# Performance work log

Measured on AMD Instinct MI355X. Metric: run time of the kernel, lower is better.

The kernel has to match this reference:

```python
import jax, jax.numpy as jnp
import numpy as np
import math

B, S = 512, 50
L, U = 40000, 20000
D_MODEL, D_LOC, D_USR, D_T, H, D_FF = 80, 56, 12, 12, 4, 160
DH = D_MODEL // H


def _layernorm(x, g, b, eps=1e-5):
    m = x.mean(-1, keepdims=True)
    v = ((x - m) ** 2).mean(-1, keepdims=True)
    return (x - m) / jnp.sqrt(v + eps) * g + b


def setup_inputs() -> dict:
    key = jax.random.key(0)
    ks = jax.random.split(key, 16)
    loc_seq = jax.random.randint(ks[0], (B, S), 0, L)
    user_seq = jax.random.randint(ks[1], (B, S), 0, U)
    weekday_seq = jax.random.randint(ks[2], (B, S), 0, 7)
    start_min_seq = jax.random.uniform(ks[3], (B, S), jnp.float32, 0.0, 1440.0)
    dur_seq = jax.random.uniform(ks[4], (B, S), jnp.float32, 0.0, 600.0)
    diff_seq = jax.random.randint(ks[5], (B, S), 0, 7)
    mask = jnp.ones((B, S), dtype=bool)
    # sinusoidal positional-encoding buffer (60, 80), as in __init__
    pos = np.arange(60, dtype=np.float32)[:, None]
    div = np.exp(np.arange(0, D_MODEL, 2, dtype=np.float32) * (-math.log(10000.0) / D_MODEL))
    pe = np.zeros((60, D_MODEL), dtype=np.float32)
    pe[:, 0::2] = np.sin(pos * div)
    pe[:, 1::2] = np.cos(pos * div)
    g = lambda k, shape: jax.random.normal(k, shape, jnp.float32) * 0.02
    return dict(
        loc_seq=loc_seq, user_seq=user_seq, weekday_seq=weekday_seq,
        start_min_seq=start_min_seq, dur_seq=dur_seq, diff_seq=diff_seq, mask=mask,
        loc_emb=jax.random.normal(ks[6], (L, D_LOC), jnp.float32) * 0.01,
        user_emb=jax.random.normal(ks[7], (U, D_USR), jnp.float32) * 0.01,
        tproj_w=g(ks[8], (6, D_T)), tproj_b=jnp.zeros((D_T,), jnp.float32),
        in_norm_g=jnp.ones((D_MODEL,), jnp.float32), in_norm_b=jnp.zeros((D_MODEL,), jnp.float32),
        attn_in_w=g(ks[9], (3 * D_MODEL, D_MODEL)), attn_in_b=jnp.zeros((3 * D_MODEL,), jnp.float32),
        attn_out_w=g(ks[10], (D_MODEL, D_MODEL)), attn_out_b=jnp.zeros((D_MODEL,), jnp.float32),
        norm1_g=jnp.ones((D_MODEL,), jnp.float32), norm1_b=jnp.zeros((D_MODEL,), jnp.float32),
        ff_w1=g(ks[11], (D_MODEL, D_FF)), ff_b1=jnp.zeros((D_FF,), jnp.float32),
        ff_w2=g(ks[12], (D_FF, D_MODEL)), ff_b2=jnp.zeros((D_MODEL,), jnp.float32),
        norm2_g=jnp.ones((D_MODEL,), jnp.float32), norm2_b=jnp.zeros((D_MODEL,), jnp.float32),
        pred_w1=g(ks[13], (D_MODEL, D_FF)), pred_b1=jnp.zeros((D_FF,), jnp.float32),
        pred_w2=g(ks[14], (D_FF, L)), pred_b2=jnp.zeros((L,), jnp.float32),
        recency_decay=jnp.float32(0.62), freq_weight=jnp.float32(2.2),
        history_scale=jnp.float32(11.0), model_weight=jnp.float32(0.22),
        pe=jnp.asarray(pe),
    )


def _history_scores(loc_seq, mask, recency_decay, freq_weight, history_scale):
    # Vectorized scatter-max (recency) + scatter-add (frequency) over the whole
    # (B, S) index set -- replaces the per-timestep python loop of the original.
    maskf = mask.astype(jnp.float32)
    time_from_end = jnp.arange(S - 1, -1, -1, dtype=jnp.float32)  # seq_len - t - 1
    rw = jnp.power(recency_decay, time_from_end)[None, :] * maskf  # (B, S)
    bidx = jnp.broadcast_to(jnp.arange(B)[:, None], (B, S))
    rec = jnp.zeros((B, L), jnp.float32).at[bidx, loc_seq].max(rw)
    freq = jnp.zeros((B, L), jnp.float32).at[bidx, loc_seq].add(maskf)
    freq = freq / jnp.clip(freq.max(axis=1, keepdims=True), 1.0)
    return history_scale * (rec + freq_weight * freq)


def _forward(loc_seq, user_seq, weekday_seq, start_min_seq, dur_seq, diff_seq, mask,
             loc_emb, user_emb, tproj_w, tproj_b, in_norm_g, in_norm_b,
             attn_in_w, attn_in_b, attn_out_w, attn_out_b, norm1_g, norm1_b,
             ff_w1, ff_b1, ff_w2, ff_b2, norm2_g, norm2_b,
             pred_w1, pred_b1, pred_w2, pred_b2,
             recency_decay, freq_weight, history_scale, model_weight, pe):
    hist = _history_scores(loc_seq, mask, recency_decay, freq_weight, history_scale)
    le = loc_emb[loc_seq]                       # (B, S, 56)
    ue = user_emb[user_seq]                     # (B, S, 12)
    tr = (start_min_seq / 60.0) / 24.0 * 2.0 * jnp.pi
    wr = weekday_seq.astype(jnp.float32) / 7.0 * 2.0 * jnp.pi
    tf = jnp.stack([jnp.sin(tr), jnp.cos(tr), jnp.log1p(dur_seq) / 8.0,
                    jnp.sin(wr), jnp.cos(wr), diff_seq.astype(jnp.float32) / 7.0], axis=-1)
    te = tf @ tproj_w + tproj_b                 # (B, S, 12)
    x = jnp.concatenate([le, ue, te], axis=-1)  # (B, S, 80)
    x = _layernorm(x, in_norm_g, in_norm_b)
    x = x + pe[:S][None]
    # multi-head self-attention with key padding mask (dropout=eval mode)
    qkv = x @ attn_in_w.T + attn_in_b
    q, k, v = jnp.split(qkv, 3, axis=-1)
    q = q.reshape(B, S, H, DH)
    k = k.reshape(B, S, H, DH)
    v = v.reshape(B, S, H, DH)
    scores = jnp.einsum('bqhd,bkhd->bhqk', q, k) / jnp.sqrt(jnp.float32(DH))
    scores = jnp.where(mask[:, None, None, :], scores, -jnp.inf)
    attn = jax.nn.softmax(scores, axis=-1)
    ao = jnp.einsum('bhqk,bkhd->bqhd', attn, v).reshape(B, S, D_MODEL)
    ao = ao @ attn_out_w.T + attn_out_b
    x = _layernorm(x + ao, norm1_g, norm1_b)
    ff = jax.nn.gelu(x @ ff_w1 + ff_b1, approximate=False) @ ff_w2 + ff_b2
    x = _layernorm(x + ff, norm2_g, norm2_b)
    seq_lens = mask.sum(axis=1) - 1             # index of last valid token
    last = jnp.take_along_axis(x, seq_lens[:, None, None], axis=1)[:, 0]  # (B, 80)
    logits = jax.nn.gelu(last @ pred_w1 + pred_b1, approximate=False) @ pred_w2 + pred_b2
    return hist + model_weight * (jax.nn.softmax(logits, axis=1) * L)


def reference(loc_seq, user_seq, weekday_seq, start_min_seq, dur_seq, diff_seq, mask,
              loc_emb, user_emb, tproj_w, tproj_b, in_norm_g, in_norm_b,
              attn_in_w, attn_in_b, attn_out_w, attn_out_b, norm1_g, norm1_b,
              ff_w1, ff_b1, ff_w2, ff_b2, norm2_g, norm2_b,
              pred_w1, pred_b1, pred_w2, pred_b2,
              recency_decay, freq_weight, history_scale, model_weight, pe):
    return _forward(loc_seq, user_seq, weekday_seq, start_min_seq, dur_seq, diff_seq, mask,
                    loc_emb, user_emb, tproj_w, tproj_b, in_norm_g, in_norm_b,
                    attn_in_w, attn_in_b, attn_out_w, attn_out_b, norm1_g, norm1_b,
                    ff_w1, ff_b1, ff_w2, ff_b2, norm2_g, norm2_b,
                    pred_w1, pred_b1, pred_w2, pred_b2,
                    recency_decay, freq_weight, history_scale, model_weight, pe)
```

## Files before the change

kernel.cpp:

```cpp
#include <hip/hip_runtime.h>
#include <math.h>

#define BB 512
#define SS 50
#define LL 40000
#define DM 80
#define DLOC 56
#define DUSR 12
#define HH 4
#define DH 20
#define DFF 160

typedef __attribute__((ext_vector_type(8))) short short8v;
typedef __attribute__((ext_vector_type(4))) float f32x4;

__device__ __forceinline__ unsigned short f2bf(float f) {
    unsigned u = __float_as_uint(f);
    u += 0x7fffu + ((u >> 16) & 1u);
    return (unsigned short)(u >> 16);
}

__device__ __forceinline__ float gelu_exact(float x) {
    return 0.5f * x * (1.0f + erff(x * 0.70710678118654752f));
}

__global__ __launch_bounds__(256) void k_fused(
        const int* __restrict__ loc_seq, const int* __restrict__ user_seq,
        const int* __restrict__ wd_seq, const float* __restrict__ start_seq,
        const float* __restrict__ dur_seq, const int* __restrict__ diff_seq,
        const float* __restrict__ loc_emb, const float* __restrict__ user_emb,
        const float* __restrict__ tproj_w, const float* __restrict__ tproj_b,
        const float* __restrict__ in_g, const float* __restrict__ in_b,
        const float* __restrict__ pe,
        const float* __restrict__ Wqkv, const float* __restrict__ bqkv,
        const float* __restrict__ aw, const float* __restrict__ ab,
        const float* __restrict__ n1g, const float* __restrict__ n1b,
        const float* __restrict__ w1, const float* __restrict__ b1,
        const float* __restrict__ w2, const float* __restrict__ b2,
        const float* __restrict__ n2g, const float* __restrict__ n2b,
        const float* __restrict__ pw1, const float* __restrict__ pb1,
        const float* __restrict__ p_decay, const float* __restrict__ p_fw,
        const float* __restrict__ p_hs,
        float* __restrict__ histval, int* __restrict__ histloc,
        unsigned short* __restrict__ gvec, float* __restrict__ rowsum) {
    int b = blockIdx.x, tid = threadIdx.x;
    int w = tid >> 6, ln = tid & 63;
    __shared__ __align__(16) float xs[SS][DM];
    __shared__ float xsT[DM][SS];
    __shared__ float tf6[SS][6];
    __shared__ float rw[SS];
    __shared__ int   loc[SS];
    __shared__ int   usr[SS];
    __shared__ float qr[DM];
    __shared__ float uu[HH][DM];
    __shared__ float scw[HH][SS];
    __shared__ float wsm[HH][DM];
    __shared__ float ao[DM];
    __shared__ float v1[DM];
    __shared__ float v2[DM];
    __shared__ float f1[DFF];
    __shared__ float stat[2];

    if (tid == 0) rowsum[b] = 0.f;

    if (tid < SS) {
        int t = tid;
        loc[t] = loc_seq[b * SS + t];
        usr[t] = user_seq[b * SS + t];
        float tr = start_seq[b * SS + t] * (float)(M_PI / 720.0);
        float wrd = (float)wd_seq[b * SS + t] * (float)(2.0 * M_PI / 7.0);
        tf6[t][0] = sinf(tr); tf6[t][1] = cosf(tr);
        tf6[t][2] = log1pf(dur_seq[b * SS + t]) * 0.125f;
        tf6[t][3] = sinf(wrd); tf6[t][4] = cosf(wrd);
        tf6[t][5] = (float)diff_seq[b * SS + t] * (1.f / 7.f);
        rw[t] = exp2f((float)(SS - 1 - t) * log2f(p_decay[0]));
    }
    __syncthreads();

    for (int idx = tid; idx < SS * DM; idx += 256) {
        int t = idx / DM, d = idx - t * DM;
        float v;
        if (d < DLOC) {
            v = loc_emb[(size_t)loc[t] * DLOC + d];
        } else if (d < DLOC + DUSR) {
            v = user_emb[(size_t)usr[t] * DUSR + (d - DLOC)];
        } else {
            int j = d - (DLOC + DUSR);
            float a = tproj_b[j];
            #pragma unroll
            for (int i = 0; i < 6; ++i) a += tf6[t][i] * tproj_w[i * 12 + j];
            v = a;
        }
        xs[t][d] = v;
    }
    __syncthreads();

    for (int t = w; t < SS; t += 4) {
        float a0 = xs[t][ln];
        float a1 = (ln < 16) ? xs[t][64 + ln] : 0.f;
        float sm = a0 + a1;
        #pragma unroll
        for (int m = 1; m < 64; m <<= 1) sm += __shfl_xor(sm, m);
        float mean = sm * (1.f / DM);
        float d0 = a0 - mean, d1 = (ln < 16) ? (a1 - mean) : 0.f;
        float vs = d0 * d0 + d1 * d1;
        #pragma unroll
        for (int m = 1; m < 64; m <<= 1) vs += __shfl_xor(vs, m);
        float inv = rsqrtf(vs * (1.f / DM) + 1e-5f);
        float r0 = d0 * inv * in_g[ln] + in_b[ln] + pe[t * DM + ln];
        xs[t][ln] = r0; xsT[ln][t] = r0;
        if (ln < 16) {
            float r1 = d1 * inv * in_g[64 + ln] + in_b[64 + ln] + pe[t * DM + 64 + ln];
            xs[t][64 + ln] = r1; xsT[64 + ln][t] = r1;
        }
    }
    __syncthreads();

    if (w == 0) {
        int t = ln;
        int c = 0; float rmx = 0.f; int first = (t < SS) ? 1 : 0;
        if (t < SS) {
            int my = loc[t];
            for (int j = 0; j < SS; ++j) {
                if (loc[j] == my) {
                    c++; rmx = fmaxf(rmx, rw[j]);
                    if (j < t) first = 0;
                }
            }
        }
        int mc = c;
        #pragma unroll
        for (int m = 1; m < 64; m <<= 1) mc = max(mc, __shfl_xor(mc, m));
        if (t < SS) {
            float val = 0.f;
            if (first) val = p_hs[0] * (rmx + p_fw[0] * ((float)c / (float)max(mc, 1)));
            histval[b * SS + t] = val;
            histloc[b * SS + t] = loc[t];
        }
    } else if (tid >= 64 && tid < 64 + DM) {
        int j = tid - 64;
        const float* Wr = Wqkv + (size_t)j * DM;
        float a = bqkv[j];
        for (int d = 0; d < DM; ++d) a += xs[49][d] * Wr[d];
        qr[j] = a;
    }
    __syncthreads();

    {
        int idx = tid;
        float a0 = 0.f, a1 = 0.f;
        int h0 = idx / DM, d0i = idx - h0 * DM;
        #pragma unroll 4
        for (int j = 0; j < DH; ++j)
            a0 += qr[h0 * DH + j] * Wqkv[(size_t)(DM + h0 * DH + j) * DM + d0i];
        int idx1 = tid + 256;
        int h1 = idx1 / DM, d1i = idx1 - h1 * DM;
        if (tid < 64) {
            #pragma unroll 4
            for (int j = 0; j < DH; ++j)
                a1 += qr[h1 * DH + j] * Wqkv[(size_t)(DM + h1 * DH + j) * DM + d1i];
        }
        uu[h0][d0i] = a0;
        if (tid < 64) uu[h1][d1i] = a1;
    }
    __syncthreads();

    if (tid < HH * SS) {
        int h = tid / SS, s = tid - h * SS;
        float a = 0.f;
        #pragma unroll 4
        for (int d = 0; d < DM; ++d) a += uu[h][d] * xsT[d][s];
        scw[h][s] = a * 0.22360679774997896f;
    }
    __syncthreads();

    {
        float v = (ln < SS) ? scw[w][ln] : -1e30f;
        float m = v;
        #pragma unroll
        for (int mk = 1; mk < 64; mk <<= 1) m = fmaxf(m, __shfl_xor(m, mk));
        float e = (ln < SS) ? __expf(v - m) : 0.f;
        float sm = e;
        #pragma unroll
        for (int mk = 1; mk < 64; mk <<= 1) sm += __shfl_xor(sm, mk);
        if (ln < SS) scw[w][ln] = e / sm;
    }
    __syncthreads();

    {
        int idx = tid;
        int h0 = idx / DM, d0i = idx - h0 * DM;
        float a0 = 0.f, a1 = 0.f;
        #pragma unroll 5
        for (int s = 0; s < SS; ++s) a0 += scw[h0][s] * xs[s][d0i];
        int idx1 = tid + 256;
        int h1 = idx1 / DM, d1i = idx1 - h1 * DM;
        if (tid < 64) {
            #pragma unroll 5
            for (int s = 0; s < SS; ++s) a1 += scw[h1][s] * xs[s][d1i];
        }
        wsm[h0][d0i] = a0;
        if (tid < 64) wsm[h1][d1i] = a1;
    }
    __syncthreads();

    if (tid < DM) {
        int h = tid / DH;
        const float* Wr = Wqkv + (size_t)(2 * DM + tid) * DM;
        float a = bqkv[2 * DM + tid];
        for (int d = 0; d < DM; ++d) a += Wr[d] * wsm[h][d];
        ao[tid] = a;
    }
    __syncthreads();

    if (tid < DM) {
        float a = ab[tid];
        const float* ar = aw + (size_t)tid * DM;
        for (int d = 0; d < DM; ++d) a += ao[d] * ar[d];
        v1[tid] = xs[49][tid] + a;
    }
    __syncthreads();
    if (w == 0) {
        float a0 = (ln < DM) ? v1[ln] : 0.f;
        float a1 = (ln < 16) ? v1[64 + ln] : 0.f;
        float sm = a0 + a1;
        #pragma unroll
        for (int m = 1; m < 64; m <<= 1) sm += __shfl_xor(sm, m);
        float mean = sm * (1.f / DM);
        float d0 = (ln < DM) ? a0 - mean : 0.f, d1 = (ln < 16) ? a1 - mean : 0.f;
        float vs = d0 * d0 + d1 * d1;
        #pragma unroll
        for (int m = 1; m < 64; m <<= 1) vs += __shfl_xor(vs, m);
        if (ln == 0) { stat[0] = mean; stat[1] = rsqrtf(vs * (1.f / DM) + 1e-5f); }
    }
    __syncthreads();
    if (tid < DM) v2[tid] = (v1[tid] - stat[0]) * stat[1] * n1g[tid] + n1b[tid];
    __syncthreads();

    if (tid < DFF) {
        float a = b1[tid];
        for (int d = 0; d < DM; ++d) a += v2[d] * w1[(size_t)d * DFF + tid];
        f1[tid] = gelu_exact(a);
    }
    __syncthreads();

    if (tid < DM) {
        float a = b2[tid];
        for (int j = 0; j < DFF; ++j) a += f1[j] * w2[(size_t)j * DM + tid];
        v1[tid] = v2[tid] + a;
    }
    __syncthreads();
    if (w == 0) {
        float a0 = (ln < DM) ? v1[ln] : 0.f;
        float a1 = (ln < 16) ? v1[64 + ln] : 0.f;
        float sm = a0 + a1;
        #pragma unroll
        for (int m = 1; m < 64; m <<= 1) sm += __shfl_xor(sm, m);
        float mean = sm * (1.f / DM);
        float d0 = (ln < DM) ? a0 - mean : 0.f, d1 = (ln < 16) ? a1 - mean : 0.f;
        float vs = d0 * d0 + d1 * d1;
        #pragma unroll
        for (int m = 1; m < 64; m <<= 1) vs += __shfl_xor(vs, m);
        if (ln == 0) { stat[0] = mean; stat[1] = rsqrtf(vs * (1.f / DM) + 1e-5f); }
    }
    __syncthreads();
    if (tid < DM) v2[tid] = (v1[tid] - stat[0]) * stat[1] * n2g[tid] + n2b[tid];
    __syncthreads();

    if (tid < DFF) {
        float a = pb1[tid];
        for (int d = 0; d < DM; ++d) a += v2[d] * pw1[(size_t)d * DFF + tid];
        gvec[b * DFF + tid] = f2bf(gelu_exact(a));
    }
}

__global__ __launch_bounds__(256) void k_prep(const float* __restrict__ B,
                                              unsigned short* __restrict__ Bp) {
    int n = blockIdx.x * 256 + threadIdx.x;
    if (n >= LL) return;
    #pragma unroll
    for (int c = 0; c < 4; ++c) {
        int k0 = c * 40;
        unsigned pk[20];
        #pragma unroll
        for (int jj = 0; jj < 20; ++jj) {
            float lo = B[(size_t)(k0 + 2 * jj) * LL + n];
            float hi = B[(size_t)(k0 + 2 * jj + 1) * LL + n];
            pk[jj] = (unsigned)f2bf(lo) | ((unsigned)f2bf(hi) << 16);
        }
        uint4* dst = (uint4*)&Bp[(size_t)n * DFF + k0];
        #pragma unroll
        for (int q = 0; q < 5; ++q)
            dst[q] = make_uint4(pk[q * 4], pk[q * 4 + 1], pk[q * 4 + 2], pk[q * 4 + 3]);
    }
}

template<int WRITE>
__global__ __launch_bounds__(512) void k_mfma(
        const unsigned short* __restrict__ Abf,
        const unsigned short* __restrict__ Bp,
        const float* __restrict__ bias,
        const float* __restrict__ p_mw,
        float* __restrict__ rowsum,
        float* __restrict__ out) {
    int by = blockIdx.x;
    int bx = blockIdx.y;
    int m0 = by * 256, n0 = bx * 64;
    int tid = threadIdx.x;
    int l = tid & 63, w = tid >> 6;
    int lr = l & 15, lg = l >> 4;
    int wr = (w >> 1) * 64, wc = (w & 1) * 32;
    __shared__ float prs[256][2];

    f32x4 acc[4][2] = {};
    const short8v* Arow[4];
    #pragma unroll
    for (int mi = 0; mi < 4; ++mi)
        Arow[mi] = (const short8v*)&Abf[(size_t)(m0 + wr + mi * 16 + lr) * DFF];
    const short8v* B0 = (const short8v*)&Bp[(size_t)(n0 + wc + lr) * DFF];
    const short8v* B1 = (const short8v*)&Bp[(size_t)(n0 + wc + 16 + lr) * DFF];

    #pragma unroll
    for (int step = 0; step < 5; ++step) {
        int kq = step * 4 + lg;
        short8v b0 = B0[kq];
        short8v b1 = B1[kq];
        #pragma unroll
        for (int mi = 0; mi < 4; ++mi) {
            short8v a = Arow[mi][kq];
            acc[mi][0] = __builtin_amdgcn_mfma_f32_16x16x32_bf16(a, b0, acc[mi][0], 0, 0, 0);
            acc[mi][1] = __builtin_amdgcn_mfma_f32_16x16x32_bf16(a, b1, acc[mi][1], 0, 0, 0);
        }
    }
    float bia0 = bias[n0 + wc + lr];
    float bia1 = bias[n0 + wc + 16 + lr];
    if (WRITE) {
        float mwL = p_mw[0] * (float)LL;
        #pragma unroll
        for (int mi = 0; mi < 4; ++mi) {
            #pragma unroll
            for (int r = 0; r < 4; ++r) {
                int row = m0 + wr + mi * 16 + lg * 4 + r;
                float scl = mwL / rowsum[row];
                out[(size_t)row * LL + n0 + wc + lr]      = __expf(acc[mi][0][r] + bia0) * scl;
                out[(size_t)row * LL + n0 + wc + 16 + lr] = __expf(acc[mi][1][r] + bia1) * scl;
            }
        }
    } else {
        #pragma unroll
        for (int mi = 0; mi < 4; ++mi) {
            #pragma unroll
            for (int r = 0; r < 4; ++r) {
                float sv = __expf(acc[mi][0][r] + bia0) + __expf(acc[mi][1][r] + bia1);
                #pragma unroll
                for (int mk = 1; mk < 16; mk <<= 1) sv += __shfl_xor(sv, mk);
                if (lr == 0) prs[wr + mi * 16 + lg * 4 + r][w & 1] = sv;
            }
        }
        __syncthreads();
        if (tid < 256)
            atomicAdd(&rowsum[m0 + tid], prs[tid][0] + prs[tid][1]);
    }
}

__global__ void k_scatter(const float* __restrict__ histval,
                          const int* __restrict__ histloc,
                          float* __restrict__ out) {
    int b = blockIdx.x, t = threadIdx.x;
    if (t < SS) {
        float v = histval[b * SS + t];
        if (v != 0.f) atomicAdd(&out[(size_t)b * LL + histloc[b * SS + t]], v);
    }
}

extern "C" void kernel_launch(void* const* d_in, const int* in_sizes, int n_in,
                              void* d_out, int out_size, void* d_ws, size_t ws_size,
                              hipStream_t stream) {
    const int*   loc_seq   = (const int*)d_in[0];
    const int*   user_seq  = (const int*)d_in[1];
    const int*   wd_seq    = (const int*)d_in[2];
    const float* start_seq = (const float*)d_in[3];
    const float* dur_seq   = (const float*)d_in[4];
    const int*   diff_seq  = (const int*)d_in[5];
    const float* loc_emb   = (const float*)d_in[7];
    const float* user_emb  = (const float*)d_in[8];
    const float* tproj_w   = (const float*)d_in[9];
    const float* tproj_b   = (const float*)d_in[10];
    const float* in_g      = (const float*)d_in[11];
    const float* in_b      = (const float*)d_in[12];
    const float* attn_in_w = (const float*)d_in[13];
    const float* attn_in_b = (const float*)d_in[14];
    const float* attn_out_w= (const float*)d_in[15];
    const float* attn_out_b= (const float*)d_in[16];
    const float* n1g       = (const float*)d_in[17];
    const float* n1b       = (const float*)d_in[18];
    const float* ff_w1     = (const float*)d_in[19];
    const float* ff_b1     = (const float*)d_in[20];
    const float* ff_w2     = (const float*)d_in[21];
    const float* ff_b2     = (const float*)d_in[22];
    const float* n2g       = (const float*)d_in[23];
    const float* n2b       = (const float*)d_in[24];
    const float* pw1       = (const float*)d_in[25];
    const float* pb1       = (const float*)d_in[26];
    const float* pw2       = (const float*)d_in[27];
    const float* pb2       = (const float*)d_in[28];
    const float* p_decay   = (const float*)d_in[29];
    const float* p_fw      = (const float*)d_in[30];
    const float* p_hs      = (const float*)d_in[31];
    const float* p_mw      = (const float*)d_in[32];
    const float* pe        = (const float*)d_in[33];
    float* out = (float*)d_out;

    char* base = (char*)d_ws;
    unsigned short* Bp = (unsigned short*)base;
    float* rowsum  = (float*)(base + (size_t)LL * DFF * 2);
    float* histval = rowsum + 512;
    int*   histloc = (int*)(histval + 25600);
    unsigned short* gvec = (unsigned short*)(histloc + 25600);

    k_fused<<<BB, 256, 0, stream>>>(loc_seq, user_seq, wd_seq, start_seq, dur_seq,
                                    diff_seq, loc_emb, user_emb, tproj_w, tproj_b,
                                    in_g, in_b, pe, attn_in_w, attn_in_b,
                                    attn_out_w, attn_out_b, n1g, n1b,
                                    ff_w1, ff_b1, ff_w2, ff_b2, n2g, n2b,
                                    pw1, pb1, p_decay, p_fw, p_hs,
                                    histval, histloc, gvec, rowsum);
    k_prep<<<(LL + 255) / 256, 256, 0, stream>>>(pw2, Bp);
    dim3 g4(2, 625);
    k_mfma<0><<<g4, 512, 0, stream>>>(gvec, Bp, pb2, p_mw, rowsum, out);
    k_mfma<1><<<g4, 512, 0, stream>>>(gvec, Bp, pb2, p_mw, rowsum, out);
    k_scatter<<<BB, 64, 0, stream>>>(histval, histloc, out);
}
```

Baseline: 279.8 us.

## Merge weight prep into front kernel and switch to k-major bf16 operand layout

```diff
diff --git a/kernel.cpp b/kernel.cpp
--- a/kernel.cpp
+++ b/kernel.cpp
@@ -10,6 +10,8 @@
 #define HH 4
 #define DH 20
 #define DFF 160
+#define XP 81
+#define NPREP 157
 
 typedef __attribute__((ext_vector_type(8))) short short8v;
 typedef __attribute__((ext_vector_type(4))) float f32x4;
@@ -24,7 +26,7 @@
     return 0.5f * x * (1.0f + erff(x * 0.70710678118654752f));
 }
 
-__global__ __launch_bounds__(256) void k_fused(
+__global__ __launch_bounds__(256) void k_front(
         const int* __restrict__ loc_seq, const int* __restrict__ user_seq,
         const int* __restrict__ wd_seq, const float* __restrict__ start_seq,
         const float* __restrict__ dur_seq, const int* __restrict__ diff_seq,
@@ -39,14 +41,32 @@
         const float* __restrict__ w2, const float* __restrict__ b2,
         const float* __restrict__ n2g, const float* __restrict__ n2b,
         const float* __restrict__ pw1, const float* __restrict__ pb1,
+        const float* __restrict__ pw2,
         const float* __restrict__ p_decay, const float* __restrict__ p_fw,
         const float* __restrict__ p_hs,
         float* __restrict__ histval, int* __restrict__ histloc,
-        unsigned short* __restrict__ gvec, float* __restrict__ rowsum) {
-    int b = blockIdx.x, tid = threadIdx.x;
-    int w = tid >> 6, ln = tid & 63;
-    __shared__ __align__(16) float xs[SS][DM];
-    __shared__ float xsT[DM][SS];
+        unsigned short* __restrict__ gvec, unsigned short* __restrict__ Bp,
+        float* __restrict__ rowsum) {
+    int tid = threadIdx.x;
+
+    if (blockIdx.x >= BB) {
+        int n = (blockIdx.x - BB) * 256 + tid;
+        if (n < LL) {
+            #pragma unroll
+            for (int kq = 0; kq < 20; ++kq) {
+                unsigned short pk[8];
+                #pragma unroll
+                for (int j = 0; j < 8; ++j)
+                    pk[j] = f2bf(pw2[(size_t)(kq * 8 + j) * LL + n]);
+                *(uint4*)&Bp[((size_t)kq * LL + n) * 8] = *(const uint4*)pk;
+            }
+        }
+        return;
+    }
+
+    int b = blockIdx.x;
+    int w = tid >> 6, l = tid & 63;
+    __shared__ float xs[SS][XP];
     __shared__ float tf6[SS][6];
     __shared__ float rw[SS];
     __shared__ int   loc[SS];
@@ -59,7 +79,6 @@
     __shared__ float v1[DM];
     __shared__ float v2[DM];
     __shared__ float f1[DFF];
-    __shared__ float stat[2];
 
     if (tid == 0) rowsum[b] = 0.f;
 
@@ -77,47 +96,25 @@
     }
     __syncthreads();
 
-    for (int idx = tid; idx < SS * DM; idx += 256) {
-        int t = idx / DM, d = idx - t * DM;
-        float v;
-        if (d < DLOC) {
-            v = loc_emb[(size_t)loc[t] * DLOC + d];
-        } else if (d < DLOC + DUSR) {
-            v = user_emb[(size_t)usr[t] * DUSR + (d - DLOC)];
-        } else {
-            int j = d - (DLOC + DUSR);
-            float a = tproj_b[j];
-            #pragma unroll
-            for (int i = 0; i < 6; ++i) a += tf6[t][i] * tproj_w[i * 12 + j];
-            v = a;
-        }
-        xs[t][d] = v;
-    }
-    __syncthreads();
-
-    for (int t = w; t < SS; t += 4) {
-        float a0 = xs[t][ln];
-        float a1 = (ln < 16) ? xs[t][64 + ln] : 0.f;
-        float sm = a0 + a1;
-        #pragma unroll
-        for (int m = 1; m < 64; m <<= 1) sm += __shfl_xor(sm, m);
-        float mean = sm * (1.f / DM);
-        float d0 = a0 - mean, d1 = (ln < 16) ? (a1 - mean) : 0.f;
-        float vs = d0 * d0 + d1 * d1;
-        #pragma unroll
-        for (int m = 1; m < 64; m <<= 1) vs += __shfl_xor(vs, m);
-        float inv = rsqrtf(vs * (1.f / DM) + 1e-5f);
-        float r0 = d0 * inv * in_g[ln] + in_b[ln] + pe[t * DM + ln];
-        xs[t][ln] = r0; xsT[ln][t] = r0;
-        if (ln < 16) {
-            float r1 = d1 * inv * in_g[64 + ln] + in_b[64 + ln] + pe[t * DM + 64 + ln];
-            xs[t][64 + ln] = r1; xsT[64 + ln][t] = r1;
-        }
-    }
-    __syncthreads();
-
-    if (w == 0) {
-        int t = ln;
+    if (w < 3) {
+        for (int idx = tid; idx < SS * DM; idx += 192) {
+            int t = idx / DM, d = idx - t * DM;
+            float v;
+            if (d < DLOC) {
+                v = loc_emb[(size_t)loc[t] * DLOC + d];
+            } else if (d < DLOC + DUSR) {
+                v = user_emb[(size_t)usr[t] * DUSR + (d - DLOC)];
+            } else {
+                int j = d - (DLOC + DUSR);
+                float a = tproj_b[j];
+                #pragma unroll
+                for (int i = 0; i < 6; ++i) a += tf6[t][i] * tproj_w[i * 12 + j];
+                v = a;
+            }
+            xs[t][d] = v;
+        }
+    } else {
+        int t = l;
         int c = 0; float rmx = 0.f; int first = (t < SS) ? 1 : 0;
         if (t < SS) {
             int my = loc[t];
@@ -137,104 +134,143 @@
             histval[b * SS + t] = val;
             histloc[b * SS + t] = loc[t];
         }
-    } else if (tid >= 64 && tid < 64 + DM) {
-        int j = tid - 64;
-        const float* Wr = Wqkv + (size_t)j * DM;
-        float a = bqkv[j];
-        for (int d = 0; d < DM; ++d) a += xs[49][d] * Wr[d];
-        qr[j] = a;
-    }
-    __syncthreads();
-
-    {
-        int idx = tid;
-        float a0 = 0.f, a1 = 0.f;
-        int h0 = idx / DM, d0i = idx - h0 * DM;
+    }
+    __syncthreads();
+
+    for (int t = w; t < SS; t += 4) {
+        float a0 = xs[t][l];
+        float a1 = (l < 16) ? xs[t][64 + l] : 0.f;
+        float sm = a0 + a1;
+        #pragma unroll
+        for (int m = 1; m < 64; m <<= 1) sm += __shfl_xor(sm, m);
+        float mean = sm * (1.f / DM);
+        float d0 = a0 - mean, d1 = (l < 16) ? (a1 - mean) : 0.f;
+        float vs = d0 * d0 + d1 * d1;
+        #pragma unroll
+        for (int m = 1; m < 64; m <<= 1) vs += __shfl_xor(vs, m);
+        float inv = rsqrtf(vs * (1.f / DM) + 1e-5f);
+        xs[t][l] = d0 * inv * in_g[l] + in_b[l] + pe[t * DM + l];
+        if (l < 16)
+            xs[t][64 + l] = d1 * inv * in_g[64 + l] + in_b[64 + l] + pe[t * DM + 64 + l];
+    }
+    __syncthreads();
+
+    {
+        float xl0 = xs[49][l];
+        float xl1 = (l < 16) ? xs[49][64 + l] : 0.f;
+        for (int i = 0; i < 20; ++i) {
+            int j = w * 20 + i;
+            const float* Wr = Wqkv + (size_t)j * DM;
+            float p = xl0 * Wr[l];
+            if (l < 16) p += xl1 * Wr[64 + l];
+            #pragma unroll
+            for (int m = 1; m < 64; m <<= 1) p += __shfl_xor(p, m);
+            if (l == 0) qr[j] = p + bqkv[j];
+        }
+    }
+    __syncthreads();
+
+    {
+        int h0 = tid / DM, d0i = tid - (tid / DM) * DM;
+        float a0 = 0.f;
         #pragma unroll 4
         for (int j = 0; j < DH; ++j)
             a0 += qr[h0 * DH + j] * Wqkv[(size_t)(DM + h0 * DH + j) * DM + d0i];
-        int idx1 = tid + 256;
-        int h1 = idx1 / DM, d1i = idx1 - h1 * DM;
+        uu[h0][d0i] = a0;
         if (tid < 64) {
+            int idx1 = tid + 256;
+            int h1 = idx1 / DM, d1i = idx1 - h1 * DM;
+            float a1 = 0.f;
             #pragma unroll 4
             for (int j = 0; j < DH; ++j)
                 a1 += qr[h1 * DH + j] * Wqkv[(size_t)(DM + h1 * DH + j) * DM + d1i];
-        }
-        uu[h0][d0i] = a0;
-        if (tid < 64) uu[h1][d1i] = a1;
+            uu[h1][d1i] = a1;
+        }
     }
     __syncthreads();
 
     if (tid < HH * SS) {
-        int h = tid / SS, s = tid - h * SS;
+        int h = tid / SS, s = tid - (tid / SS) * SS;
         float a = 0.f;
         #pragma unroll 4
-        for (int d = 0; d < DM; ++d) a += uu[h][d] * xsT[d][s];
+        for (int d = 0; d < DM; ++d) a += uu[h][d] * xs[s][d];
         scw[h][s] = a * 0.22360679774997896f;
     }
     __syncthreads();
 
     {
-        float v = (ln < SS) ? scw[w][ln] : -1e30f;
+        float v = (l < SS) ? scw[w][l] : -1e30f;
         float m = v;
         #pragma unroll
         for (int mk = 1; mk < 64; mk <<= 1) m = fmaxf(m, __shfl_xor(m, mk));
-        float e = (ln < SS) ? __expf(v - m) : 0.f;
+        float e = (l < SS) ? __expf(v - m) : 0.f;
         float sm = e;
         #pragma unroll
         for (int mk = 1; mk < 64; mk <<= 1) sm += __shfl_xor(sm, mk);
-        if (ln < SS) scw[w][ln] = e / sm;
-    }
-    __syncthreads();
-
-    {
-        int idx = tid;
-        int h0 = idx / DM, d0i = idx - h0 * DM;
-        float a0 = 0.f, a1 = 0.f;
+        if (l < SS) scw[w][l] = e / sm;
+    }
+    __syncthreads();
+
+    {
+        int h0 = tid / DM, d0i = tid - (tid / DM) * DM;
+        float a0 = 0.f;
         #pragma unroll 5
         for (int s = 0; s < SS; ++s) a0 += scw[h0][s] * xs[s][d0i];
-        int idx1 = tid + 256;
-        int h1 = idx1 / DM, d1i = idx1 - h1 * DM;
+        wsm[h0][d0i] = a0;
         if (tid < 64) {
+            int idx1 = tid + 256;
+            int h1 = idx1 / DM, d1i = idx1 - h1 * DM;
+            float a1 = 0.f;
             #pragma unroll 5
             for (int s = 0; s < SS; ++s) a1 += scw[h1][s] * xs[s][d1i];
-        }
-        wsm[h0][d0i] = a0;
-        if (tid < 64) wsm[h1][d1i] = a1;
-    }
-    __syncthreads();
-
-    if (tid < DM) {
-        int h = tid / DH;
-        const float* Wr = Wqkv + (size_t)(2 * DM + tid) * DM;
-        float a = bqkv[2 * DM + tid];
-        for (int d = 0; d < DM; ++d) a += Wr[d] * wsm[h][d];
-        ao[tid] = a;
-    }
-    __syncthreads();
-
-    if (tid < DM) {
-        float a = ab[tid];
-        const float* ar = aw + (size_t)tid * DM;
-        for (int d = 0; d < DM; ++d) a += ao[d] * ar[d];
-        v1[tid] = xs[49][tid] + a;
-    }
-    __syncthreads();
-    if (w == 0) {
-        float a0 = (ln < DM) ? v1[ln] : 0.f;
-        float a1 = (ln < 16) ? v1[64 + ln] : 0.f;
+            wsm[h1][d1i] = a1;
+        }
+    }
+    __syncthreads();
+
+    {
+        float wl0 = wsm[w][l];
+        float wl1 = (l < 16) ? wsm[w][64 + l] : 0.f;
+        for (int i = 0; i < 20; ++i) {
+            int j = w * 20 + i;
+            const float* Wr = Wqkv + (size_t)(2 * DM + j) * DM;
+            float p = wl0 * Wr[l];
+            if (l < 16) p += wl1 * Wr[64 + l];
+            #pragma unroll
+            for (int m = 1; m < 64; m <<= 1) p += __shfl_xor(p, m);
+            if (l == 0) ao[j] = p + bqkv[2 * DM + j];
+        }
+    }
+    __syncthreads();
+
+    {
+        float al0 = ao[l];
+        float al1 = (l < 16) ? ao[64 + l] : 0.f;
+        for (int i = 0; i < 20; ++i) {
+            int j = w * 20 + i;
+            const float* Wr = aw + (size_t)j * DM;
+            float p = al0 * Wr[l];
+            if (l < 16) p += al1 * Wr[64 + l];
+            #pragma unroll
+            for (int m = 1; m < 64; m <<= 1) p += __shfl_xor(p, m);
+            if (l == 0) v1[j] = xs[49][j] + p + ab[j];
+        }
+    }
+    __syncthreads();
+
+    {
+        float a0 = v1[l], a1 = (l < 16) ? v1[64 + l] : 0.f;
         float sm = a0 + a1;
         #pragma unroll
         for (int m = 1; m < 64; m <<= 1) sm += __shfl_xor(sm, m);
         float mean = sm * (1.f / DM);
-        float d0 = (ln < DM) ? a0 - mean : 0.f, d1 = (ln < 16) ? a1 - mean : 0.f;
+        float d0 = a0 - mean, d1 = (l < 16) ? (a1 - mean) : 0.f;
         float vs = d0 * d0 + d1 * d1;
         #pragma unroll
         for (int m = 1; m < 64; m <<= 1) vs += __shfl_xor(vs, m);
-        if (ln == 0) { stat[0] = mean; stat[1] = rsqrtf(vs * (1.f / DM) + 1e-5f); }
-    }
-    __syncthreads();
-    if (tid < DM) v2[tid] = (v1[tid] - stat[0]) * stat[1] * n1g[tid] + n1b[tid];
+        float inv = rsqrtf(vs * (1.f / DM) + 1e-5f);
+        if (tid < DM) v2[tid] = (v1[tid] - mean) * inv * n1g[tid] + n1b[tid];
+    }
     __syncthreads();
 
     if (tid < DFF) {
@@ -250,48 +286,26 @@
         v1[tid] = v2[tid] + a;
     }
     __syncthreads();
-    if (w == 0) {
-        float a0 = (ln < DM) ? v1[ln] : 0.f;
-        float a1 = (ln < 16) ? v1[64 + ln] : 0.f;
+
+    {
+        float a0 = v1[l], a1 = (l < 16) ? v1[64 + l] : 0.f;
         float sm = a0 + a1;
         #pragma unroll
         for (int m = 1; m < 64; m <<= 1) sm += __shfl_xor(sm, m);
         float mean = sm * (1.f / DM);
-        float d0 = (ln < DM) ? a0 - mean : 0.f, d1 = (ln < 16) ? a1 - mean : 0.f;
+        float d0 = a0 - mean, d1 = (l < 16) ? (a1 - mean) : 0.f;
         float vs = d0 * d0 + d1 * d1;
         #pragma unroll
         for (int m = 1; m < 64; m <<= 1) vs += __shfl_xor(vs, m);
-        if (ln == 0) { stat[0] = mean; stat[1] = rsqrtf(vs * (1.f / DM) + 1e-5f); }
-    }
-    __syncthreads();
-    if (tid < DM) v2[tid] = (v1[tid] - stat[0]) * stat[1] * n2g[tid] + n2b[tid];
+        float inv = rsqrtf(vs * (1.f / DM) + 1e-5f);
+        if (tid < DM) v2[tid] = (v1[tid] - mean) * inv * n2g[tid] + n2b[tid];
+    }
     __syncthreads();
 
     if (tid < DFF) {
         float a = pb1[tid];
         for (int d = 0; d < DM; ++d) a += v2[d] * pw1[(size_t)d * DFF + tid];
-        gvec[b * DFF + tid] = f2bf(gelu_exact(a));
-    }
-}
-
-__global__ __launch_bounds__(256) void k_prep(const float* __restrict__ B,
-                                              unsigned short* __restrict__ Bp) {
-    int n = blockIdx.x * 256 + threadIdx.x;
-    if (n >= LL) return;
-    #pragma unroll
-    for (int c = 0; c < 4; ++c) {
-        int k0 = c * 40;
-        unsigned pk[20];
-        #pragma unroll
-        for (int jj = 0; jj < 20; ++jj) {
-            float lo = B[(size_t)(k0 + 2 * jj) * LL + n];
-            float hi = B[(size_t)(k0 + 2 * jj + 1) * LL + n];
-            pk[jj] = (unsigned)f2bf(lo) | ((unsigned)f2bf(hi) << 16);
-        }
-        uint4* dst = (uint4*)&Bp[(size_t)n * DFF + k0];
-        #pragma unroll
-        for (int q = 0; q < 5; ++q)
-            dst[q] = make_uint4(pk[q * 4], pk[q * 4 + 1], pk[q * 4 + 2], pk[q * 4 + 3]);
+        gvec[((size_t)(tid >> 3) * BB + b) * 8 + (tid & 7)] = f2bf(gelu_exact(a));
     }
 }
 
@@ -312,22 +326,17 @@
     int wr = (w >> 1) * 64, wc = (w & 1) * 32;
     __shared__ float prs[256][2];
 
+    const short8v* Af = (const short8v*)Abf;
+    const short8v* Bf = (const short8v*)Bp;
     f32x4 acc[4][2] = {};
-    const short8v* Arow[4];
-    #pragma unroll
-    for (int mi = 0; mi < 4; ++mi)
-        Arow[mi] = (const short8v*)&Abf[(size_t)(m0 + wr + mi * 16 + lr) * DFF];
-    const short8v* B0 = (const short8v*)&Bp[(size_t)(n0 + wc + lr) * DFF];
-    const short8v* B1 = (const short8v*)&Bp[(size_t)(n0 + wc + 16 + lr) * DFF];
-
     #pragma unroll
     for (int step = 0; step < 5; ++step) {
         int kq = step * 4 + lg;
-        short8v b0 = B0[kq];
-        short8v b1 = B1[kq];
+        short8v b0 = Bf[(size_t)kq * LL + n0 + wc + lr];
+        short8v b1 = Bf[(size_t)kq * LL + n0 + wc + 16 + lr];
         #pragma unroll
         for (int mi = 0; mi < 4; ++mi) {
-            short8v a = Arow[mi][kq];
+            short8v a = Af[kq * BB + m0 + wr + mi * 16 + lr];
             acc[mi][0] = __builtin_amdgcn_mfma_f32_16x16x32_bf16(a, b0, acc[mi][0], 0, 0, 0);
             acc[mi][1] = __builtin_amdgcn_mfma_f32_16x16x32_bf16(a, b1, acc[mi][1], 0, 0, 0);
         }
@@ -418,14 +427,14 @@
     int*   histloc = (int*)(histval + 25600);
     unsigned short* gvec = (unsigned short*)(histloc + 25600);
 
-    k_fused<<<BB, 256, 0, stream>>>(loc_seq, user_seq, wd_seq, start_seq, dur_seq,
-                                    diff_seq, loc_emb, user_emb, tproj_w, tproj_b,
-                                    in_g, in_b, pe, attn_in_w, attn_in_b,
-                                    attn_out_w, attn_out_b, n1g, n1b,
-                                    ff_w1, ff_b1, ff_w2, ff_b2, n2g, n2b,
-                                    pw1, pb1, p_decay, p_fw, p_hs,
-                                    histval, histloc, gvec, rowsum);
-    k_prep<<<(LL + 255) / 256, 256, 0, stream>>>(pw2, Bp);
+    k_front<<<BB + NPREP, 256, 0, stream>>>(loc_seq, user_seq, wd_seq, start_seq,
+                                            dur_seq, diff_seq, loc_emb, user_emb,
+                                            tproj_w, tproj_b, in_g, in_b, pe,
+                                            attn_in_w, attn_in_b, attn_out_w, attn_out_b,
+                                            n1g, n1b, ff_w1, ff_b1, ff_w2, ff_b2,
+                                            n2g, n2b, pw1, pb1, pw2,
+                                            p_decay, p_fw, p_hs,
+                                            histval, histloc, gvec, Bp, rowsum);
     dim3 g4(2, 625);
     k_mfma<0><<<g4, 512, 0, stream>>>(gvec, Bp, pb2, p_mw, rowsum, out);
     k_mfma<1><<<g4, 512, 0, stream>>>(gvec, Bp, pb2, p_mw, rowsum, out);
```

Result: slower. 303.2 us (+8.3%).
